# Performance work log

Measured on AMD Instinct MI355X. Metric: run time of the kernel, lower is better.

The kernel has to match this reference:

```python
import jax, jax.numpy as jnp
import numpy as np

# MiniCPM-style decode-step config (matches init_kwargs)
L, B, H, HKV, D, S, HID, FF = 8, 4, 16, 8, 64, 2048, 1024, 2816
SCALE_DEPTH = 1.4
ROPE_THETA = 10000.0
EPS = 1e-5


def _rms(x, w):
    v = jnp.mean(jnp.square(x), axis=-1, keepdims=True)
    return x * jax.lax.rsqrt(v + EPS) * w


def _rotate_half(x):
    x1, x2 = jnp.split(x, 2, axis=-1)
    return jnp.concatenate([-x2, x1], axis=-1)


def setup_inputs() -> dict:
    key = jax.random.key(0)
    ks = jax.random.split(key, 12)
    s = lambda i, shape, fan: jax.random.normal(ks[i], shape, jnp.float32) / np.sqrt(fan)
    return {
        "x": jax.random.normal(ks[0], (B, HID), jnp.float32),
        "k_cache": jax.random.normal(ks[1], (L, B, HKV, S, D), jnp.float32),
        "v_cache": jax.random.normal(ks[2], (L, B, HKV, S, D), jnp.float32),
        "Wq": s(3, (L, HID, H * D), HID),
        "Wk": s(4, (L, HID, HKV * D), HID),
        "Wv": s(5, (L, HID, HKV * D), HID),
        "Wo": s(6, (L, H * D, HID), H * D),
        "Wgate": s(7, (L, HID, FF), HID),
        "Wup": s(8, (L, HID, FF), HID),
        "Wdown": s(9, (L, FF, HID), FF),
        "norm1_w": jnp.ones((L, HID), jnp.float32),
        "norm2_w": jnp.ones((L, HID), jnp.float32),
        "final_norm_w": jnp.ones((HID,), jnp.float32),
        "current_length": 1500,
    }


def reference(x, k_cache, v_cache, Wq, Wk, Wv, Wo, Wgate, Wup, Wdown,
              norm1_w, norm2_w, final_norm_w, current_length):
    pos = jnp.asarray(current_length, jnp.int32)
    # RoPE for the single new position (rope_emb(position_id))
    inv_freq = 1.0 / (ROPE_THETA ** (jnp.arange(0, D, 2, dtype=jnp.float32) / D))
    ang = pos.astype(jnp.float32) * inv_freq            # [D/2]
    cos = jnp.concatenate([jnp.cos(ang), jnp.cos(ang)])  # [D]
    sin = jnp.concatenate([jnp.sin(ang), jnp.sin(ang)])
    positions = jnp.arange(S)
    write_mask = (positions == pos)[None, None, :, None]  # [1,1,S,1]
    valid = (positions <= pos)                            # [S]
    mup = SCALE_DEPTH / np.sqrt(L)
    g = H // HKV

    def layer(h, params):
        wq, wk, wv, wo, wg, wu, wd, n1, n2, kc, vc = params
        hn = _rms(h, n1)
        q = (hn @ wq).reshape(B, HKV, g, 1, D)   # grouped query heads
        k = (hn @ wk).reshape(B, HKV, 1, D)
        v = (hn @ wv).reshape(B, HKV, 1, D)
        q = q * cos + _rotate_half(q) * sin
        k = k * cos + _rotate_half(k) * sin
        # broadcast 'where' write into the full static cache (faithful to source)
        ak = jnp.where(write_mask, k, kc)         # [B,HKV,S,D]
        av = jnp.where(write_mask, v, vc)
        scores = jnp.einsum('bhgqd,bhsd->bhgqs', q, ak) / np.sqrt(D)
        scores = jnp.where(valid[None, None, None, None, :], scores, -jnp.inf)
        p = jax.nn.softmax(scores, axis=-1)
        o = jnp.einsum('bhgqs,bhsd->bhgqd', p, av).reshape(B, H * D)
        h = h + (o @ wo) * mup
        hn2 = _rms(h, n2)
        m = (jax.nn.silu(hn2 @ wg) * (hn2 @ wu)) @ wd
        h = h + m * mup
        return h, (k, v)  # one-position K/V updates [B,HKV,1,D]

    xs = (Wq, Wk, Wv, Wo, Wgate, Wup, Wdown, norm1_w, norm2_w, k_cache, v_cache)
    h, (k_upd, v_upd) = jax.lax.scan(layer, x, xs)
    h = _rms(h, final_norm_w)
    return h, k_upd, v_upd, pos + 1
```

## Files before the change

kernel.cpp:

```cpp
#include <hip/hip_runtime.h>

#define L_   8
#define B_   4
#define H_   16
#define HKV_ 8
#define D_   64
#define S_   2048
#define HID_ 1024
#define FF_  2816
#define EPS_ 1e-5f
#define MUP_ 0.49497474683058327f
#define SCALE_ 0.125f
#define NCH_ 32

#define OUT_H   0
#define OUT_K   4096
#define OUT_V   (4096 + 16384)
#define OUT_POS (4096 + 16384 + 16384)

enum {
  WS_HC  = 0,
  WS_QP  = 4096,
  WS_AM  = WS_QP + 262144,
  WS_AL  = WS_AM + 2048,
  WS_AO  = WS_AL + 2048,
  WS_GP  = WS_AO + 131072,
  WS_UP  = WS_GP + 360448,
  WS_END = WS_UP + 360448
};

__device__ __forceinline__ int read_pos_dev(const int* p) {
  int v = p[0];
  if (v >= 0 && v < S_) return v;
  float f = __int_as_float(v);
  if (f >= 0.0f && f <= (float)(S_ - 1)) return (int)(f + 0.5f);
  return 1500;
}

__device__ __forceinline__ float wave_sum(float v) {
  for (int m = 1; m < 64; m <<= 1) v += __shfl_xor(v, m);
  return v;
}
__device__ __forceinline__ float wave_max(float v) {
  for (int m = 1; m < 64; m <<= 1) v = fmaxf(v, __shfl_xor(v, m));
  return v;
}

__device__ __forceinline__ void rms_of(const float* hsrc, float* red, float* rs) {
  int t = threadIdx.x;
  float part[4] = {0.f, 0.f, 0.f, 0.f};
  #pragma unroll
  for (int j = 0; j < 4; ++j) {
    int c2 = t + j * 256;
    #pragma unroll
    for (int b = 0; b < 4; ++b) {
      float v = hsrc[b * HID_ + c2];
      part[b] += v * v;
    }
  }
  int w = t >> 6;
  #pragma unroll
  for (int b = 0; b < 4; ++b) {
    float s = wave_sum(part[b]);
    if ((t & 63) == 0) red[w * 4 + b] = s;
  }
  __syncthreads();
  #pragma unroll
  for (int b = 0; b < 4; ++b)
    rs[b] = rsqrtf((red[b] + red[4 + b] + red[8 + b] + red[12 + b]) * (1.0f / HID_) + EPS_);
}

__global__ void __launch_bounds__(256)
k1_qkv(const float* __restrict__ Wq, const float* __restrict__ Wk,
       const float* __restrict__ Wv, const float* __restrict__ n1,
       const float* __restrict__ x, float* __restrict__ ws, int l) {
  int cb = blockIdx.x & 7, kc = blockIdx.x >> 3;
  int t = threadIdx.x;
  int col = cb * 256 + t;
  const float* W; int wcol, stride;
  if (col < 1024)      { W = Wq + (size_t)l * HID_ * 1024; wcol = col;        stride = 1024; }
  else if (col < 1536) { W = Wk + (size_t)l * HID_ * 512;  wcol = col - 1024; stride = 512;  }
  else                 { W = Wv + (size_t)l * HID_ * 512;  wcol = col - 1536; stride = 512;  }
  const float* wp = W + (size_t)(kc * 32) * stride + wcol;
  float wv[32];
  #pragma unroll
  for (int i = 0; i < 32; ++i) wv[i] = wp[(size_t)i * stride];

  const float* hsrc = (l == 0) ? x : (ws + WS_HC);
  __shared__ float red[16];
  __shared__ __align__(16) float xs[4][32];
  float rs[4];
  rms_of(hsrc, red, rs);
  if (l == 0 && blockIdx.x < 4) {
    for (int j = 0; j < 4; ++j) {
      int c2 = t + j * 256;
      ws[WS_HC + blockIdx.x * HID_ + c2] = x[blockIdx.x * HID_ + c2];
    }
  }
  if (t < 128) {
    int b = t >> 5, i = t & 31;
    int gc = kc * 32 + i;
    xs[b][i] = hsrc[b * HID_ + gc] * rs[b] * n1[l * HID_ + gc];
  }
  __syncthreads();
  float a0 = 0.f, a1 = 0.f, a2 = 0.f, a3 = 0.f;
  #pragma unroll
  for (int i = 0; i < 32; ++i) {
    float w_ = wv[i];
    a0 += w_ * xs[0][i]; a1 += w_ * xs[1][i];
    a2 += w_ * xs[2][i]; a3 += w_ * xs[3][i];
  }
  ws[WS_QP + ((size_t)kc * 4 + 0) * 2048 + col] = a0;
  ws[WS_QP + ((size_t)kc * 4 + 1) * 2048 + col] = a1;
  ws[WS_QP + ((size_t)kc * 4 + 2) * 2048 + col] = a2;
  ws[WS_QP + ((size_t)kc * 4 + 3) * 2048 + col] = a3;
}

__global__ void __launch_bounds__(256)
k2_attn(const float* __restrict__ kcache, const float* __restrict__ vcache,
        const int* __restrict__ posp, float* __restrict__ ws,
        float* __restrict__ out, int l) {
  int bh = blockIdx.x >> 5, ns = blockIdx.x & 31;
  int b = bh >> 3, kv = bh & 7;
  int t = threadIdx.x;
  int w = t >> 6, lane = t & 63, r = lane >> 4, c = lane & 15;
  int pos = read_pos_dev(posp);
  int s0 = ns * 64;
  if (s0 > pos) {
    if (t == 0) {
      int base = ((b * HKV_ + kv) * 2) * NCH_ + ns;
      ws[WS_AM + base] = -1e30f;       ws[WS_AM + base + NCH_] = -1e30f;
      ws[WS_AL + base] = 0.f;          ws[WS_AL + base + NCH_] = 0.f;
    }
    return;
  }
  __shared__ __align__(16) float Kst[64 * 68];
  __shared__ __align__(16) float Vst[64 * 68];
  __shared__ __align__(16) float qL[2][64];
  __shared__ __align__(16) float knL[64], vnL[64];
  __shared__ float rawL[256], sc0[64], sc1[64], red[8];
  __shared__ __align__(16) float oacc[2][4][64];

  const float* Kb = kcache + (((size_t)l * B_ + b) * HKV_ + kv) * S_ * 64;
  const float* Vb = vcache + (((size_t)l * B_ + b) * HKV_ + kv) * S_ * 64;

  {
    const float4* Ksrc = (const float4*)(Kb + (size_t)s0 * 64);
    const float4* Vsrc = (const float4*)(Vb + (size_t)s0 * 64);
    #pragma unroll
    for (int i = 0; i < 4; ++i) {
      int f4 = t + i * 256;
      int row = f4 >> 4, c4 = f4 & 15;
      float4 kk = Ksrc[f4];
      float4 vv = Vsrc[f4];
      *(float4*)&Kst[row * 68 + 4 * c4] = kk;
      *(float4*)&Vst[row * 68 + 4 * c4] = vv;
    }
  }

  int cg;
  if (t < 128)      cg = (kv * 2 + (t >> 6)) * 64 + (t & 63);
  else if (t < 192) cg = 1024 + kv * 64 + (t & 63);
  else              cg = 1536 + kv * 64 + (t & 63);
  float s = 0.f;
  #pragma unroll
  for (int q = 0; q < 32; ++q) s += ws[WS_QP + ((size_t)q * 4 + b) * 2048 + cg];
  rawL[t] = s;
  __syncthreads();
  {
    int dd = t & 63;
    if (t < 192) {
      int idx = dd & 31;
      float inv = expf(-(float)idx * (1.0f / 32.0f) * 9.210340371976184f);
      float ang = (float)pos * inv;
      float sn, cs; __sincosf(ang, &sn, &cs);
      float partner = rawL[t ^ 32];
      float rot = (dd < 32) ? -partner : partner;
      float v = rawL[t] * cs + rot * sn;
      if (t < 128) qL[t >> 6][dd] = v;
      else {
        knL[dd] = v;
        if (ns == 0) out[OUT_K + (((size_t)l * B_ + b) * HKV_ + kv) * 64 + dd] = v;
      }
    } else {
      vnL[dd] = rawL[t];
      if (ns == 0) out[OUT_V + (((size_t)l * B_ + b) * HKV_ + kv) * 64 + dd] = rawL[t];
    }
  }
  __syncthreads();
  if (pos >= s0 && pos < s0 + 64) {
    int row = pos - s0;
    if (t < 64)                Kst[row * 68 + t] = knL[t];
    else if (t < 128)          Vst[row * 68 + (t - 64)] = vnL[t - 64];
  }
  __syncthreads();

  float4 q0 = *(float4*)&qL[0][4 * c];
  float4 q1 = *(float4*)&qL[1][4 * c];
  #pragma unroll
  for (int it = 0; it < 4; ++it) {
    int row = it * 16 + w * 4 + r;
    int sp = s0 + row;
    float4 k4 = *(float4*)&Kst[row * 68 + 4 * c];
    float d0 = k4.x * q0.x + k4.y * q0.y + k4.z * q0.z + k4.w * q0.w;
    float d1 = k4.x * q1.x + k4.y * q1.y + k4.z * q1.z + k4.w * q1.w;
    #pragma unroll
    for (int m = 1; m <= 8; m <<= 1) { d0 += __shfl_xor(d0, m); d1 += __shfl_xor(d1, m); }
    if (c == 0) {
      bool valid = (sp <= pos);
      sc0[row] = valid ? d0 * SCALE_ : -1e30f;
      sc1[row] = valid ? d1 * SCALE_ : -1e30f;
    }
  }
  __syncthreads();
  float v0 = (t < 64) ? sc0[t] : -1e30f;
  float v1 = (t < 64) ? sc1[t] : -1e30f;
  float m0 = wave_max(v0), m1 = wave_max(v1);
  if (lane == 0) { red[w] = m0; red[4 + w] = m1; }
  __syncthreads();
  m0 = fmaxf(fmaxf(red[0], red[1]), fmaxf(red[2], red[3]));
  m1 = fmaxf(fmaxf(red[4], red[5]), fmaxf(red[6], red[7]));
  float e0 = (t < 64) ? expf(v0 - m0) : 0.f;
  float e1 = (t < 64) ? expf(v1 - m1) : 0.f;
  __syncthreads();
  if (t < 64) { sc0[t] = e0; sc1[t] = e1; }
  float se0 = wave_sum(e0), se1 = wave_sum(e1);
  if (lane == 0) { red[w] = se0; red[4 + w] = se1; }
  __syncthreads();
  if (t == 0) {
    int base = ((b * HKV_ + kv) * 2) * NCH_ + ns;
    ws[WS_AM + base] = m0;          ws[WS_AM + base + NCH_] = m1;
    ws[WS_AL + base] = red[0] + red[1] + red[2] + red[3];
    ws[WS_AL + base + NCH_] = red[4] + red[5] + red[6] + red[7];
  }
  float4 a0 = make_float4(0.f, 0.f, 0.f, 0.f);
  float4 a1 = make_float4(0.f, 0.f, 0.f, 0.f);
  #pragma unroll
  for (int it = 0; it < 4; ++it) {
    int row = it * 16 + w * 4 + r;
    float4 v4 = *(float4*)&Vst[row * 68 + 4 * c];
    float p0 = sc0[row], p1 = sc1[row];
    a0.x += p0 * v4.x; a0.y += p0 * v4.y; a0.z += p0 * v4.z; a0.w += p0 * v4.w;
    a1.x += p1 * v4.x; a1.y += p1 * v4.y; a1.z += p1 * v4.z; a1.w += p1 * v4.w;
  }
  #pragma unroll
  for (int m = 16; m <= 32; m <<= 1) {
    a0.x += __shfl_xor(a0.x, m); a0.y += __shfl_xor(a0.y, m);
    a0.z += __shfl_xor(a0.z, m); a0.w += __shfl_xor(a0.w, m);
    a1.x += __shfl_xor(a1.x, m); a1.y += __shfl_xor(a1.y, m);
    a1.z += __shfl_xor(a1.z, m); a1.w += __shfl_xor(a1.w, m);
  }
  if (r == 0) {
    *(float4*)&oacc[0][w][4 * c] = a0;
    *(float4*)&oacc[1][w][4 * c] = a1;
  }
  __syncthreads();
  if (t < 64) {
    float r0 = oacc[0][0][t] + oacc[0][1][t] + oacc[0][2][t] + oacc[0][3][t];
    float r1 = oacc[1][0][t] + oacc[1][1][t] + oacc[1][2][t] + oacc[1][3][t];
    int h0 = kv * 2;
    ws[WS_AO + ((size_t)(b * H_ + h0)     * NCH_ + ns) * 64 + t] = r0;
    ws[WS_AO + ((size_t)(b * H_ + h0 + 1) * NCH_ + ns) * 64 + t] = r1;
  }
}

__global__ void __launch_bounds__(256)
k3_oproj(const float* __restrict__ Wo, float* __restrict__ ws, int l) {
  int cb = blockIdx.x & 3, kc = blockIdx.x >> 2;
  int t = threadIdx.x;
  int col = cb * 256 + t;
  const float* wp = Wo + ((size_t)l * HID_ + kc * 16) * HID_ + col;
  float wv[16];
  #pragma unroll
  for (int i = 0; i < 16; ++i) wv[i] = wp[(size_t)i * HID_];

  __shared__ __align__(16) float oT[16][4];
  if (t < 64) {
    int jj = t >> 2, bb = t & 3;
    int dim = kc * 16 + jj, h = dim >> 6, d = dim & 63;
    int mb = ((bb * HKV_ + (h >> 1)) * 2 + (h & 1)) * NCH_;
    float mx = -1e30f;
    #pragma unroll
    for (int n = 0; n < NCH_; ++n) mx = fmaxf(mx, ws[WS_AM + mb + n]);
    float ls = 0.f, os = 0.f;
    #pragma unroll
    for (int n = 0; n < NCH_; ++n) {
      float wg = expf(ws[WS_AM + mb + n] - mx);
      ls += wg * ws[WS_AL + mb + n];
      os += wg * ws[WS_AO + ((size_t)(bb * H_ + h) * NCH_ + n) * 64 + d];
    }
    oT[jj][bb] = os / ls;
  }
  __syncthreads();
  float a0 = 0.f, a1 = 0.f, a2 = 0.f, a3 = 0.f;
  #pragma unroll
  for (int i = 0; i < 16; ++i) {
    float w_ = wv[i];
    float4 o4 = *(float4*)&oT[i][0];
    a0 += w_ * o4.x; a1 += w_ * o4.y; a2 += w_ * o4.z; a3 += w_ * o4.w;
  }
  atomicAdd(ws + WS_HC + 0 * HID_ + col, MUP_ * a0);
  atomicAdd(ws + WS_HC + 1 * HID_ + col, MUP_ * a1);
  atomicAdd(ws + WS_HC + 2 * HID_ + col, MUP_ * a2);
  atomicAdd(ws + WS_HC + 3 * HID_ + col, MUP_ * a3);
}

__global__ void __launch_bounds__(256)
k4_gateup(const float* __restrict__ Wg, const float* __restrict__ Wu,
          const float* __restrict__ n2, float* __restrict__ ws, int l) {
  int cb = blockIdx.x % 11, kc = blockIdx.x / 11;
  int t = threadIdx.x;
  int col = cb * 256 + t;
  const float* wgp = Wg + ((size_t)l * HID_ + kc * 32) * FF_ + col;
  const float* wup = Wu + ((size_t)l * HID_ + kc * 32) * FF_ + col;
  float gv[32], uv[32];
  #pragma unroll
  for (int i = 0; i < 32; ++i) { gv[i] = wgp[(size_t)i * FF_]; uv[i] = wup[(size_t)i * FF_]; }

  const float* hsrc = ws + WS_HC;
  __shared__ float red[16];
  __shared__ __align__(16) float xs[4][32];
  float rs[4];
  rms_of(hsrc, red, rs);
  if (t < 128) {
    int b = t >> 5, i = t & 31;
    int gc = kc * 32 + i;
    xs[b][i] = hsrc[b * HID_ + gc] * rs[b] * n2[l * HID_ + gc];
  }
  __syncthreads();
  float g0 = 0.f, g1 = 0.f, g2 = 0.f, g3 = 0.f;
  float u0 = 0.f, u1 = 0.f, u2 = 0.f, u3 = 0.f;
  #pragma unroll
  for (int i = 0; i < 32; ++i) {
    float g = gv[i], u = uv[i];
    float x0 = xs[0][i], x1 = xs[1][i], x2 = xs[2][i], x3 = xs[3][i];
    g0 += g * x0; g1 += g * x1; g2 += g * x2; g3 += g * x3;
    u0 += u * x0; u1 += u * x1; u2 += u * x2; u3 += u * x3;
  }
  ws[WS_GP + ((size_t)kc * 4 + 0) * FF_ + col] = g0;
  ws[WS_GP + ((size_t)kc * 4 + 1) * FF_ + col] = g1;
  ws[WS_GP + ((size_t)kc * 4 + 2) * FF_ + col] = g2;
  ws[WS_GP + ((size_t)kc * 4 + 3) * FF_ + col] = g3;
  ws[WS_UP + ((size_t)kc * 4 + 0) * FF_ + col] = u0;
  ws[WS_UP + ((size_t)kc * 4 + 1) * FF_ + col] = u1;
  ws[WS_UP + ((size_t)kc * 4 + 2) * FF_ + col] = u2;
  ws[WS_UP + ((size_t)kc * 4 + 3) * FF_ + col] = u3;
}

__global__ void __launch_bounds__(256)
k5_down(const float* __restrict__ Wd, float* __restrict__ ws, int l) {
  int cb = blockIdx.x & 3, kc = blockIdx.x >> 2;
  int t = threadIdx.x;
  int col = cb * 256 + t;
  const float* wp = Wd + ((size_t)l * FF_ + kc * 32) * HID_ + col;
  float wv[32];
  #pragma unroll
  for (int i = 0; i < 32; ++i) wv[i] = wp[(size_t)i * HID_];

  __shared__ __align__(16) float mT[32][4];
  if (t < 128) {
    int jj = t >> 2, bb = t & 3;
    int f = kc * 32 + jj;
    float g = 0.f, u = 0.f;
    #pragma unroll
    for (int k2 = 0; k2 < 32; ++k2) {
      g += ws[WS_GP + ((size_t)k2 * 4 + bb) * FF_ + f];
      u += ws[WS_UP + ((size_t)k2 * 4 + bb) * FF_ + f];
    }
    float sig = 1.f / (1.f + expf(-g));
    mT[jj][bb] = g * sig * u;
  }
  __syncthreads();
  float a0 = 0.f, a1 = 0.f, a2 = 0.f, a3 = 0.f;
  #pragma unroll
  for (int i = 0; i < 32; ++i) {
    float w_ = wv[i];
    float4 m4 = *(float4*)&mT[i][0];
    a0 += w_ * m4.x; a1 += w_ * m4.y; a2 += w_ * m4.z; a3 += w_ * m4.w;
  }
  atomicAdd(ws + WS_HC + 0 * HID_ + col, MUP_ * a0);
  atomicAdd(ws + WS_HC + 1 * HID_ + col, MUP_ * a1);
  atomicAdd(ws + WS_HC + 2 * HID_ + col, MUP_ * a2);
  atomicAdd(ws + WS_HC + 3 * HID_ + col, MUP_ * a3);
}

__global__ void __launch_bounds__(256)
k6_final(const float* __restrict__ fw, const int* __restrict__ posp,
         float* __restrict__ ws, float* __restrict__ out) {
  int b = blockIdx.x, t = threadIdx.x;
  __shared__ float red[4];
  float hv[4];
  float part = 0.f;
  for (int j = 0; j < 4; ++j) {
    float v = ws[WS_HC + b * HID_ + t + j * 256];
    hv[j] = v; part += v * v;
  }
  part = wave_sum(part);
  if ((t & 63) == 0) red[t >> 6] = part;
  __syncthreads();
  float rs = rsqrtf((red[0] + red[1] + red[2] + red[3]) * (1.0f / HID_) + EPS_);
  for (int j = 0; j < 4; ++j) {
    int c2 = t + j * 256;
    out[OUT_H + b * HID_ + c2] = hv[j] * rs * fw[c2];
  }
  if (b == 0 && t == 0) out[OUT_POS] = (float)(read_pos_dev(posp) + 1);
}

extern "C" void kernel_launch(void* const* d_in, const int* in_sizes, int n_in,
                              void* d_out, int out_size, void* d_ws, size_t ws_size,
                              hipStream_t stream) {
  const float* x   = (const float*)d_in[0];
  const float* kcp = (const float*)d_in[1];
  const float* vcp = (const float*)d_in[2];
  const float* Wq  = (const float*)d_in[3];
  const float* Wk  = (const float*)d_in[4];
  const float* Wv  = (const float*)d_in[5];
  const float* Wo  = (const float*)d_in[6];
  const float* Wg  = (const float*)d_in[7];
  const float* Wu  = (const float*)d_in[8];
  const float* Wd  = (const float*)d_in[9];
  const float* n1  = (const float*)d_in[10];
  const float* n2  = (const float*)d_in[11];
  const float* fw  = (const float*)d_in[12];
  const int*   pos = (const int*)d_in[13];
  float* ws  = (float*)d_ws;
  float* out = (float*)d_out;

  for (int l = 0; l < L_; ++l) {
    k1_qkv   <<< 256, 256, 0, stream>>>(Wq, Wk, Wv, n1, x, ws, l);
    k2_attn  <<<1024, 256, 0, stream>>>(kcp, vcp, pos, ws, out, l);
    k3_oproj <<< 256, 256, 0, stream>>>(Wo, ws, l);
    k4_gateup<<< 352, 256, 0, stream>>>(Wg, Wu, n2, ws, l);
    k5_down  <<< 352, 256, 0, stream>>>(Wd, ws, l);
  }
  k6_final<<<4, 256, 0, stream>>>(fw, pos, ws, out);
}
```

Before: 324.4 us.

## Prefetch next kernel's weights and KV cache into L2 from the preceding kernel

Each kernel now issues dummy loads, one per 64-byte cache line, covering the data the next kernel in the chain will read: k1 touches the K/V cache tiles for attention, k2 touches Wo, k3 touches Wgate/Wup, k4 touches Wdown, and k5 touches the next layer's Wq/Wk/Wv. An empty asm keeps the loaded values alive so the compiler does not remove the loads. The aim is to warm L2/MALL so the following launch finds its data in cache and hides the DRAM latency of a memory-bound decode step. The cost is extra memory traffic and register pressure inside each kernel. If the cache cannot hold the prefetched data until the next kernel runs, the loads are wasted.

Measured after the change: 320.7 us. About the same (-1.1%).

```diff
diff --git a/kernel.cpp b/kernel.cpp
--- a/kernel.cpp
+++ b/kernel.cpp
@@ -45,6 +45,7 @@
   for (int m = 1; m < 64; m <<= 1) v = fmaxf(v, __shfl_xor(v, m));
   return v;
 }
+__device__ __forceinline__ void keepf(float v) { asm volatile("" :: "v"(v)); }
 
 __device__ __forceinline__ void rms_of(const float* hsrc, float* red, float* rs) {
   int t = threadIdx.x;
@@ -73,7 +74,9 @@
 __global__ void __launch_bounds__(256)
 k1_qkv(const float* __restrict__ Wq, const float* __restrict__ Wk,
        const float* __restrict__ Wv, const float* __restrict__ n1,
-       const float* __restrict__ x, float* __restrict__ ws, int l) {
+       const float* __restrict__ x, const float* __restrict__ kcache,
+       const float* __restrict__ vcache, const int* __restrict__ posp,
+       float* __restrict__ ws, int l) {
   int cb = blockIdx.x & 7, kc = blockIdx.x >> 3;
   int t = threadIdx.x;
   int col = cb * 256 + t;
@@ -102,6 +105,23 @@
     int gc = kc * 32 + i;
     xs[b][i] = hsrc[b * HID_ + gc] * rs[b] * n1[l * HID_ + gc];
   }
+
+  int pos = read_pos_dev(posp);
+  float pf[8];
+  {
+    int row = t >> 2, off = (t & 3) * 16;
+    #pragma unroll
+    for (int m = 0; m < 4; ++m) {
+      int j = blockIdx.x + m * 256;
+      int bh2 = j >> 5, ns2 = j & 31;
+      int s02 = ns2 * 64;
+      bool act = (s02 <= pos);
+      size_t base = (((size_t)l * B_ + (bh2 >> 3)) * HKV_ + (bh2 & 7)) * S_ * 64
+                  + (size_t)(s02 + row) * 64 + off;
+      pf[2 * m + 0] = act ? kcache[base] : 0.f;
+      pf[2 * m + 1] = act ? vcache[base] : 0.f;
+    }
+  }
   __syncthreads();
   float a0 = 0.f, a1 = 0.f, a2 = 0.f, a3 = 0.f;
   #pragma unroll
@@ -114,24 +134,35 @@
   ws[WS_QP + ((size_t)kc * 4 + 1) * 2048 + col] = a1;
   ws[WS_QP + ((size_t)kc * 4 + 2) * 2048 + col] = a2;
   ws[WS_QP + ((size_t)kc * 4 + 3) * 2048 + col] = a3;
+  #pragma unroll
+  for (int m = 0; m < 8; ++m) keepf(pf[m]);
 }
 
 __global__ void __launch_bounds__(256)
 k2_attn(const float* __restrict__ kcache, const float* __restrict__ vcache,
-        const int* __restrict__ posp, float* __restrict__ ws,
-        float* __restrict__ out, int l) {
+        const int* __restrict__ posp, const float* __restrict__ Wo,
+        float* __restrict__ ws, float* __restrict__ out, int l) {
   int bh = blockIdx.x >> 5, ns = blockIdx.x & 31;
   int b = bh >> 3, kv = bh & 7;
   int t = threadIdx.x;
   int w = t >> 6, lane = t & 63, r = lane >> 4, c = lane & 15;
   int pos = read_pos_dev(posp);
   int s0 = ns * 64;
+
+  float pfo = 0.f;
+  if (blockIdx.x < 256) {
+    int cb3 = blockIdx.x & 3, kc3 = blockIdx.x >> 2;
+    int r3 = t >> 4, c3 = (t & 15) * 16;
+    pfo = Wo[((size_t)l * HID_ + kc3 * 16 + r3) * HID_ + cb3 * 256 + c3];
+  }
+
   if (s0 > pos) {
     if (t == 0) {
       int base = ((b * HKV_ + kv) * 2) * NCH_ + ns;
       ws[WS_AM + base] = -1e30f;       ws[WS_AM + base + NCH_] = -1e30f;
       ws[WS_AL + base] = 0.f;          ws[WS_AL + base + NCH_] = 0.f;
     }
+    keepf(pfo);
     return;
   }
   __shared__ __align__(16) float Kst[64 * 68];
@@ -262,10 +293,12 @@
     ws[WS_AO + ((size_t)(b * H_ + h0)     * NCH_ + ns) * 64 + t] = r0;
     ws[WS_AO + ((size_t)(b * H_ + h0 + 1) * NCH_ + ns) * 64 + t] = r1;
   }
+  keepf(pfo);
 }
 
 __global__ void __launch_bounds__(256)
-k3_oproj(const float* __restrict__ Wo, float* __restrict__ ws, int l) {
+k3_oproj(const float* __restrict__ Wo, const float* __restrict__ Wg,
+         const float* __restrict__ Wu, float* __restrict__ ws, int l) {
   int cb = blockIdx.x & 3, kc = blockIdx.x >> 2;
   int t = threadIdx.x;
   int col = cb * 256 + t;
@@ -291,6 +324,25 @@
     }
     oT[jj][bb] = os / ls;
   }
+
+  float pf[8];
+  {
+    #pragma unroll
+    for (int rg = 0; rg < 2; ++rg) {
+      int j = blockIdx.x + rg * 256;
+      bool act = (j < 352);
+      int jj2 = act ? j : 0;
+      int cb4 = jj2 % 11, kc4 = jj2 / 11;
+      #pragma unroll
+      for (int q = 0; q < 2; ++q) {
+        int m = t + q * 256;
+        int r4 = m >> 4, c4 = (m & 15) * 16;
+        size_t o4 = ((size_t)l * HID_ + kc4 * 32 + r4) * FF_ + cb4 * 256 + c4;
+        pf[rg * 4 + q * 2 + 0] = act ? Wg[o4] : 0.f;
+        pf[rg * 4 + q * 2 + 1] = act ? Wu[o4] : 0.f;
+      }
+    }
+  }
   __syncthreads();
   float a0 = 0.f, a1 = 0.f, a2 = 0.f, a3 = 0.f;
   #pragma unroll
@@ -303,11 +355,14 @@
   atomicAdd(ws + WS_HC + 1 * HID_ + col, MUP_ * a1);
   atomicAdd(ws + WS_HC + 2 * HID_ + col, MUP_ * a2);
   atomicAdd(ws + WS_HC + 3 * HID_ + col, MUP_ * a3);
+  #pragma unroll
+  for (int m = 0; m < 8; ++m) keepf(pf[m]);
 }
 
 __global__ void __launch_bounds__(256)
 k4_gateup(const float* __restrict__ Wg, const float* __restrict__ Wu,
-          const float* __restrict__ n2, float* __restrict__ ws, int l) {
+          const float* __restrict__ Wd, const float* __restrict__ n2,
+          float* __restrict__ ws, int l) {
   int cb = blockIdx.x % 11, kc = blockIdx.x / 11;
   int t = threadIdx.x;
   int col = cb * 256 + t;
@@ -327,6 +382,17 @@
     int gc = kc * 32 + i;
     xs[b][i] = hsrc[b * HID_ + gc] * rs[b] * n2[l * HID_ + gc];
   }
+
+  float pf[2];
+  {
+    int cb5 = blockIdx.x & 3, kc5 = blockIdx.x >> 2;
+    #pragma unroll
+    for (int q = 0; q < 2; ++q) {
+      int m = t + q * 256;
+      int r5 = m >> 4, c5 = (m & 15) * 16;
+      pf[q] = Wd[((size_t)l * FF_ + kc5 * 32 + r5) * HID_ + cb5 * 256 + c5];
+    }
+  }
   __syncthreads();
   float g0 = 0.f, g1 = 0.f, g2 = 0.f, g3 = 0.f;
   float u0 = 0.f, u1 = 0.f, u2 = 0.f, u3 = 0.f;
@@ -345,10 +411,13 @@
   ws[WS_UP + ((size_t)kc * 4 + 1) * FF_ + col] = u1;
   ws[WS_UP + ((size_t)kc * 4 + 2) * FF_ + col] = u2;
   ws[WS_UP + ((size_t)kc * 4 + 3) * FF_ + col] = u3;
+  keepf(pf[0]); keepf(pf[1]);
 }
 
 __global__ void __launch_bounds__(256)
-k5_down(const float* __restrict__ Wd, float* __restrict__ ws, int l) {
+k5_down(const float* __restrict__ Wd, const float* __restrict__ Wq,
+        const float* __restrict__ Wk, const float* __restrict__ Wv,
+        float* __restrict__ ws, int l) {
   int cb = blockIdx.x & 3, kc = blockIdx.x >> 2;
   int t = threadIdx.x;
   int col = cb * 256 + t;
@@ -370,6 +439,22 @@
     float sig = 1.f / (1.f + expf(-g));
     mT[jj][bb] = g * sig * u;
   }
+
+  float pf[2] = {0.f, 0.f};
+  if (l + 1 < L_ && blockIdx.x < 256) {
+    int cb1 = blockIdx.x & 7, kc1 = blockIdx.x >> 3;
+    #pragma unroll
+    for (int q = 0; q < 2; ++q) {
+      int m = t + q * 256;
+      int r1 = m >> 4, c1 = (m & 15) * 16;
+      int pcol = cb1 * 256 + c1;
+      const float* W1; int wcol1, stride1;
+      if (pcol < 1024)      { W1 = Wq + (size_t)(l + 1) * HID_ * 1024; wcol1 = pcol;        stride1 = 1024; }
+      else if (pcol < 1536) { W1 = Wk + (size_t)(l + 1) * HID_ * 512;  wcol1 = pcol - 1024; stride1 = 512;  }
+      else                  { W1 = Wv + (size_t)(l + 1) * HID_ * 512;  wcol1 = pcol - 1536; stride1 = 512;  }
+      pf[q] = W1[(size_t)(kc1 * 32 + r1) * stride1 + wcol1];
+    }
+  }
   __syncthreads();
   float a0 = 0.f, a1 = 0.f, a2 = 0.f, a3 = 0.f;
   #pragma unroll
@@ -382,6 +467,7 @@
   atomicAdd(ws + WS_HC + 1 * HID_ + col, MUP_ * a1);
   atomicAdd(ws + WS_HC + 2 * HID_ + col, MUP_ * a2);
   atomicAdd(ws + WS_HC + 3 * HID_ + col, MUP_ * a3);
+  keepf(pf[0]); keepf(pf[1]);
 }
 
 __global__ void __launch_bounds__(256)
@@ -427,11 +513,11 @@
   float* out = (float*)d_out;
 
   for (int l = 0; l < L_; ++l) {
-    k1_qkv   <<< 256, 256, 0, stream>>>(Wq, Wk, Wv, n1, x, ws, l);
-    k2_attn  <<<1024, 256, 0, stream>>>(kcp, vcp, pos, ws, out, l);
-    k3_oproj <<< 256, 256, 0, stream>>>(Wo, ws, l);
-    k4_gateup<<< 352, 256, 0, stream>>>(Wg, Wu, n2, ws, l);
-    k5_down  <<< 352, 256, 0, stream>>>(Wd, ws, l);
+    k1_qkv   <<< 256, 256, 0, stream>>>(Wq, Wk, Wv, n1, x, kcp, vcp, pos, ws, l);
+    k2_attn  <<<1024, 256, 0, stream>>>(kcp, vcp, pos, Wo, ws, out, l);
+    k3_oproj <<< 256, 256, 0, stream>>>(Wo, Wg, Wu, ws, l);
+    k4_gateup<<< 352, 256, 0, stream>>>(Wg, Wu, Wd, n2, ws, l);
+    k5_down  <<< 352, 256, 0, stream>>>(Wd, Wq, Wk, Wv, ws, l);
   }
   k6_final<<<4, 256, 0, stream>>>(fw, pos, ws, out);
 }
```

## Fuse all layers into one persistent cooperative megakernel with flag-based stage sync

Applied to the files above, without the earlier changes.

Replaces the 41 separate kernel launches with a single persistent 512-block kernel. Stages and layers are ordered by atomic counters in the workspace, and each stage is spin-waited on before it proceeds. Weight and KV-cache loads are issued before each wait so that memory traffic overlaps the previous stage. Per-layer workspace planes avoid write-after-read hazards, and the residual is kept in interleaved buffers. This removes launch overhead and tail bubbles, but it risks deadlock if not all blocks are resident (there is a timed-out spin) and it adds atomic contention.

After: 1.106 ms. 241% more time.

```diff
diff --git a/kernel.cpp b/kernel.cpp
--- a/kernel.cpp
+++ b/kernel.cpp
@@ -18,6 +18,481 @@
 #define OUT_V   (4096 + 16384)
 #define OUT_POS (4096 + 16384 + 16384)
 
+#define PL_QP   0
+#define PL_AM   262144
+#define PL_AL   263168
+#define PL_AO   264192
+#define PL_HCA  395264
+#define PL_HCB  399360
+#define PL_GP   403456
+#define PL_UP   763904
+#define PL_SZ   1124352
+#define FL_BASE (8 * PL_SZ)
+#define NEED_FLOATS (FL_BASE + 1024)
+#define FI(l,k) (((l) * 5 + (k)) * 16)
+
+__device__ __forceinline__ int read_pos_dev(const int* p) {
+  int v = p[0];
+  if (v >= 0 && v < S_) return v;
+  float f = __int_as_float(v);
+  if (f >= 0.0f && f <= (float)(S_ - 1)) return (int)(f + 0.5f);
+  return 1500;
+}
+__device__ __forceinline__ float wave_sum(float v) {
+  for (int m = 1; m < 64; m <<= 1) v += __shfl_xor(v, m);
+  return v;
+}
+__device__ __forceinline__ float wave_max(float v) {
+  for (int m = 1; m < 64; m <<= 1) v = fmaxf(v, __shfl_xor(v, m));
+  return v;
+}
+__device__ __forceinline__ void stg_a(float* p, float v) {
+  __hip_atomic_store(p, v, __ATOMIC_RELAXED, __HIP_MEMORY_SCOPE_AGENT);
+}
+__device__ __forceinline__ void fwait(int* flg, int idx, int target) {
+  if (threadIdx.x == 0) {
+    int n = 0;
+    while (__hip_atomic_load(flg + idx, __ATOMIC_RELAXED,
+                             __HIP_MEMORY_SCOPE_AGENT) < target) {
+      __builtin_amdgcn_s_sleep(32);
+      if (++n > (1 << 22)) break;
+    }
+  }
+  __syncthreads();
+}
+__device__ __forceinline__ void fadd(int* flg, int idx) {
+  if (threadIdx.x == 0) atomicAdd(flg + idx, 1);
+}
+
+__global__ void k_init(float* ws) {
+  int i = blockIdx.x * 256 + threadIdx.x;
+  if (i < 1024) ((int*)(ws + FL_BASE))[i] = 0;
+}
+
+__global__ void __launch_bounds__(256, 2)
+mega(const float* __restrict__ kcache, const float* __restrict__ vcache,
+     const float* __restrict__ Wq, const float* __restrict__ Wk,
+     const float* __restrict__ Wv, const float* __restrict__ Wo,
+     const float* __restrict__ Wg, const float* __restrict__ Wu,
+     const float* __restrict__ Wd, const float* __restrict__ n1,
+     const float* __restrict__ n2, const float* __restrict__ fw,
+     const float* __restrict__ x, const int* __restrict__ posp,
+     float* ws, float* out) {
+  const int bid = blockIdx.x, t = threadIdx.x;
+  int* flg = (int*)(ws + FL_BASE);
+  const int pos = read_pos_dev(posp);
+  __shared__ __align__(16) float smem[9872];
+
+  if (bid == 4 && t == 0) out[OUT_POS] = (float)(pos + 1);
+
+  #pragma unroll 1
+  for (int l = 0; l < L_; ++l) {
+    float* qp_  = ws + (size_t)l * PL_SZ + PL_QP;
+    float* am_  = ws + (size_t)l * PL_SZ + PL_AM;
+    float* al_  = ws + (size_t)l * PL_SZ + PL_AL;
+    float* ao_  = ws + (size_t)l * PL_SZ + PL_AO;
+    float* hca_ = ws + (size_t)l * PL_SZ + PL_HCA;
+    float* hcb_ = ws + (size_t)l * PL_SZ + PL_HCB;
+    float* gp_  = ws + (size_t)l * PL_SZ + PL_GP;
+    float* up_  = ws + (size_t)l * PL_SZ + PL_UP;
+
+    if (bid < 256) {
+      int cb = bid & 7, kc = bid >> 3;
+      int col = cb * 256 + t;
+      const float* W; int wcol, stride;
+      if (col < 1024)      { W = Wq + (size_t)l * HID_ * 1024; wcol = col;        stride = 1024; }
+      else if (col < 1536) { W = Wk + (size_t)l * HID_ * 512;  wcol = col - 1024; stride = 512;  }
+      else                 { W = Wv + (size_t)l * HID_ * 512;  wcol = col - 1536; stride = 512;  }
+      const float* wp = W + (size_t)(kc * 32) * stride + wcol;
+      float wv[32];
+      #pragma unroll
+      for (int i = 0; i < 32; ++i) wv[i] = wp[(size_t)i * stride];
+
+      if (l > 0) fwait(flg, FI(l - 1, 4), 352);
+
+      const float* hcbp = ws + (size_t)(l - 1) * PL_SZ + PL_HCB;
+      float4 h4[4];
+      #pragma unroll
+      for (int j = 0; j < 4; ++j) {
+        int c2 = t + j * 256;
+        if (l == 0) h4[j] = make_float4(x[c2], x[1024 + c2], x[2048 + c2], x[3072 + c2]);
+        else        h4[j] = *(const float4*)&hcbp[c2 * 4];
+      }
+      float part[4] = {0.f, 0.f, 0.f, 0.f};
+      #pragma unroll
+      for (int j = 0; j < 4; ++j) {
+        part[0] += h4[j].x * h4[j].x; part[1] += h4[j].y * h4[j].y;
+        part[2] += h4[j].z * h4[j].z; part[3] += h4[j].w * h4[j].w;
+      }
+      float* red = smem;
+      float* xs  = smem + 16;
+      int w_ = t >> 6;
+      #pragma unroll
+      for (int b = 0; b < 4; ++b) {
+        float s = wave_sum(part[b]);
+        if ((t & 63) == 0) red[w_ * 4 + b] = s;
+      }
+      __syncthreads();
+      float rs[4];
+      #pragma unroll
+      for (int b = 0; b < 4; ++b)
+        rs[b] = rsqrtf((red[b] + red[4 + b] + red[8 + b] + red[12 + b]) * (1.0f / HID_) + EPS_);
+      if (bid < 4) {
+        #pragma unroll
+        for (int j = 0; j < 4; ++j) {
+          int c2 = t + j * 256;
+          float v = (bid == 0) ? h4[j].x : (bid == 1) ? h4[j].y : (bid == 2) ? h4[j].z : h4[j].w;
+          stg_a(hca_ + c2 * 4 + bid, v);
+        }
+      }
+      if (t < 128) {
+        int b = t >> 5, i = t & 31;
+        int gc = kc * 32 + i;
+        float hval = (l == 0) ? x[b * HID_ + gc] : hcbp[gc * 4 + b];
+        xs[b * 32 + i] = hval * rs[b] * n1[l * HID_ + gc];
+      }
+      __syncthreads();
+      float a0 = 0.f, a1 = 0.f, a2 = 0.f, a3 = 0.f;
+      #pragma unroll
+      for (int i = 0; i < 32; ++i) {
+        float w = wv[i];
+        a0 += w * xs[i]; a1 += w * xs[32 + i];
+        a2 += w * xs[64 + i]; a3 += w * xs[96 + i];
+      }
+      stg_a(qp_ + ((size_t)(0 * 2048 + col)) * 32 + kc, a0);
+      stg_a(qp_ + ((size_t)(1 * 2048 + col)) * 32 + kc, a1);
+      stg_a(qp_ + ((size_t)(2 * 2048 + col)) * 32 + kc, a2);
+      stg_a(qp_ + ((size_t)(3 * 2048 + col)) * 32 + kc, a3);
+      __syncthreads();
+      fadd(flg, FI(l, 0));
+    }
+
+    {
+      int w = t >> 6, lane = t & 63, r = lane >> 4, c = lane & 15;
+      float* Kst = smem;          float* Vst = smem + 4352;
+      float* qL  = smem + 8704;   float* knL = smem + 8832;
+      float* vnL = smem + 8896;   float* rawL = smem + 8960;
+      float* sA  = smem + 9216;   float* sB  = smem + 9280;
+      float* red = smem + 9344;   float* oacc = smem + 9360;
+
+      float4 kr[4], vr[4];
+      {
+        int cid = bid, bh = cid >> 5, ns = cid & 31, s0 = ns * 64;
+        if (s0 <= pos) {
+          const float4* Ks = (const float4*)(kcache + (((size_t)l * B_ + (bh >> 3)) * HKV_ + (bh & 7)) * S_ * 64 + (size_t)s0 * 64);
+          const float4* Vs = (const float4*)(vcache + (((size_t)l * B_ + (bh >> 3)) * HKV_ + (bh & 7)) * S_ * 64 + (size_t)s0 * 64);
+          #pragma unroll
+          for (int i = 0; i < 4; ++i) { int f4 = t + i * 256; kr[i] = Ks[f4]; vr[i] = Vs[f4]; }
+        }
+      }
+      fwait(flg, FI(l, 0), 256);
+
+      #pragma unroll 1
+      for (int sub = 0; sub < 2; ++sub) {
+        int cid = bid + sub * 512;
+        int bh = cid >> 5, ns = cid & 31;
+        int b = bh >> 3, kv = bh & 7;
+        int s0 = ns * 64;
+        if (sub == 1 && s0 <= pos) {
+          const float4* Ks = (const float4*)(kcache + (((size_t)l * B_ + b) * HKV_ + kv) * S_ * 64 + (size_t)s0 * 64);
+          const float4* Vs = (const float4*)(vcache + (((size_t)l * B_ + b) * HKV_ + kv) * S_ * 64 + (size_t)s0 * 64);
+          #pragma unroll
+          for (int i = 0; i < 4; ++i) { int f4 = t + i * 256; kr[i] = Ks[f4]; vr[i] = Vs[f4]; }
+        }
+        if (s0 > pos) {
+          if (t == 0) {
+            int base = ((b * HKV_ + kv) * 2) * 32 + ns;
+            stg_a(am_ + base, -1e30f);        stg_a(am_ + base + 32, -1e30f);
+            stg_a(al_ + base, 0.f);           stg_a(al_ + base + 32, 0.f);
+          }
+        } else {
+          #pragma unroll
+          for (int i = 0; i < 4; ++i) {
+            int f4 = t + i * 256;
+            int row = f4 >> 4, c4 = f4 & 15;
+            *(float4*)&Kst[row * 68 + 4 * c4] = kr[i];
+            *(float4*)&Vst[row * 68 + 4 * c4] = vr[i];
+          }
+          int cg;
+          if (t < 128)      cg = (kv * 2 + (t >> 6)) * 64 + (t & 63);
+          else if (t < 192) cg = 1024 + kv * 64 + (t & 63);
+          else              cg = 1536 + kv * 64 + (t & 63);
+          const float* qpp = qp_ + ((size_t)(b * 2048 + cg)) * 32;
+          float s = 0.f;
+          #pragma unroll
+          for (int q = 0; q < 32; ++q) s += qpp[q];
+          rawL[t] = s;
+          __syncthreads();
+          {
+            int dd = t & 63;
+            if (t < 192) {
+              int idx = dd & 31;
+              float inv = expf(-(float)idx * (1.0f / 32.0f) * 9.210340371976184f);
+              float ang = (float)pos * inv;
+              float sn, cs; __sincosf(ang, &sn, &cs);
+              float partner = rawL[t ^ 32];
+              float rot = (dd < 32) ? -partner : partner;
+              float v = rawL[t] * cs + rot * sn;
+              if (t < 128) qL[(t >> 6) * 64 + dd] = v;
+              else {
+                knL[dd] = v;
+                if (ns == 0) out[OUT_K + (((size_t)l * B_ + b) * HKV_ + kv) * 64 + dd] = v;
+              }
+            } else {
+              vnL[dd] = rawL[t];
+              if (ns == 0) out[OUT_V + (((size_t)l * B_ + b) * HKV_ + kv) * 64 + dd] = rawL[t];
+            }
+          }
+          __syncthreads();
+          if (pos >= s0 && pos < s0 + 64) {
+            int row = pos - s0;
+            if (t < 64)       Kst[row * 68 + t] = knL[t];
+            else if (t < 128) Vst[row * 68 + (t - 64)] = vnL[t - 64];
+          }
+          __syncthreads();
+          float4 q0 = *(float4*)&qL[4 * c];
+          float4 q1 = *(float4*)&qL[64 + 4 * c];
+          #pragma unroll
+          for (int it = 0; it < 4; ++it) {
+            int row = it * 16 + w * 4 + r;
+            int sp = s0 + row;
+            float4 k4 = *(float4*)&Kst[row * 68 + 4 * c];
+            float d0 = k4.x * q0.x + k4.y * q0.y + k4.z * q0.z + k4.w * q0.w;
+            float d1 = k4.x * q1.x + k4.y * q1.y + k4.z * q1.z + k4.w * q1.w;
+            #pragma unroll
+            for (int m = 1; m <= 8; m <<= 1) { d0 += __shfl_xor(d0, m); d1 += __shfl_xor(d1, m); }
+            if (c == 0) {
+              bool valid = (sp <= pos);
+              sA[row] = valid ? d0 * SCALE_ : -1e30f;
+              sB[row] = valid ? d1 * SCALE_ : -1e30f;
+            }
+          }
+          __syncthreads();
+          float v0 = (t < 64) ? sA[t] : -1e30f;
+          float v1 = (t < 64) ? sB[t] : -1e30f;
+          float m0 = wave_max(v0), m1 = wave_max(v1);
+          if (lane == 0) { red[w] = m0; red[4 + w] = m1; }
+          __syncthreads();
+          m0 = fmaxf(fmaxf(red[0], red[1]), fmaxf(red[2], red[3]));
+          m1 = fmaxf(fmaxf(red[4], red[5]), fmaxf(red[6], red[7]));
+          float e0 = (t < 64) ? expf(v0 - m0) : 0.f;
+          float e1 = (t < 64) ? expf(v1 - m1) : 0.f;
+          __syncthreads();
+          if (t < 64) { sA[t] = e0; sB[t] = e1; }
+          float se0 = wave_sum(e0), se1 = wave_sum(e1);
+          if (lane == 0) { red[w] = se0; red[4 + w] = se1; }
+          __syncthreads();
+          if (t == 0) {
+            int base = ((b * HKV_ + kv) * 2) * 32 + ns;
+            stg_a(am_ + base, m0);          stg_a(am_ + base + 32, m1);
+            stg_a(al_ + base, red[0] + red[1] + red[2] + red[3]);
+            stg_a(al_ + base + 32, red[4] + red[5] + red[6] + red[7]);
+          }
+          float4 a0 = make_float4(0.f, 0.f, 0.f, 0.f);
+          float4 a1 = make_float4(0.f, 0.f, 0.f, 0.f);
+          #pragma unroll
+          for (int it = 0; it < 4; ++it) {
+            int row = it * 16 + w * 4 + r;
+            float4 v4 = *(float4*)&Vst[row * 68 + 4 * c];
+            float p0 = sA[row], p1 = sB[row];
+            a0.x += p0 * v4.x; a0.y += p0 * v4.y; a0.z += p0 * v4.z; a0.w += p0 * v4.w;
+            a1.x += p1 * v4.x; a1.y += p1 * v4.y; a1.z += p1 * v4.z; a1.w += p1 * v4.w;
+          }
+          #pragma unroll
+          for (int m = 16; m <= 32; m <<= 1) {
+            a0.x += __shfl_xor(a0.x, m); a0.y += __shfl_xor(a0.y, m);
+            a0.z += __shfl_xor(a0.z, m); a0.w += __shfl_xor(a0.w, m);
+            a1.x += __shfl_xor(a1.x, m); a1.y += __shfl_xor(a1.y, m);
+            a1.z += __shfl_xor(a1.z, m); a1.w += __shfl_xor(a1.w, m);
+          }
+          if (r == 0) {
+            *(float4*)&oacc[w * 64 + 4 * c] = a0;
+            *(float4*)&oacc[256 + w * 64 + 4 * c] = a1;
+          }
+          __syncthreads();
+          if (t < 64) {
+            float r0 = oacc[t] + oacc[64 + t] + oacc[128 + t] + oacc[192 + t];
+            float r1 = oacc[256 + t] + oacc[320 + t] + oacc[384 + t] + oacc[448 + t];
+            int h0 = kv * 2;
+            stg_a(ao_ + (((size_t)(b * 16 + h0))     * 64 + t) * 32 + ns, r0);
+            stg_a(ao_ + (((size_t)(b * 16 + h0 + 1)) * 64 + t) * 32 + ns, r1);
+          }
+        }
+        __syncthreads();
+      }
+      fadd(flg, FI(l, 1));
+    }
+
+    if (bid < 256) {
+      int cb = bid & 3, kc = bid >> 2;
+      int col = cb * 256 + t;
+      const float* wp = Wo + ((size_t)l * HID_ + kc * 16) * HID_ + col;
+      float wv[16];
+      #pragma unroll
+      for (int i = 0; i < 16; ++i) wv[i] = wp[(size_t)i * HID_];
+      fwait(flg, FI(l, 1), 512);
+      float* oT = smem;
+      if (t < 64) {
+        int jj = t >> 2, bb = t & 3;
+        int dim = kc * 16 + jj, h = dim >> 6, d = dim & 63;
+        const float* amp = am_ + ((bb * 8 + (h >> 1)) * 2 + (h & 1)) * 32;
+        const float* alp = al_ + ((bb * 8 + (h >> 1)) * 2 + (h & 1)) * 32;
+        const float* aop = ao_ + (((size_t)(bb * 16 + h)) * 64 + d) * 32;
+        float mx = -1e30f;
+        #pragma unroll
+        for (int n = 0; n < 32; ++n) mx = fmaxf(mx, amp[n]);
+        float ls = 0.f, os = 0.f;
+        #pragma unroll
+        for (int n = 0; n < 32; ++n) {
+          float wg = expf(amp[n] - mx);
+          ls += wg * alp[n];
+          os += wg * aop[n];
+        }
+        oT[jj * 4 + bb] = os / ls;
+      }
+      __syncthreads();
+      float a0 = 0.f, a1 = 0.f, a2 = 0.f, a3 = 0.f;
+      #pragma unroll
+      for (int i = 0; i < 16; ++i) {
+        float w = wv[i];
+        a0 += w * oT[i * 4 + 0]; a1 += w * oT[i * 4 + 1];
+        a2 += w * oT[i * 4 + 2]; a3 += w * oT[i * 4 + 3];
+      }
+      atomicAdd(hca_ + col * 4 + 0, MUP_ * a0);
+      atomicAdd(hca_ + col * 4 + 1, MUP_ * a1);
+      atomicAdd(hca_ + col * 4 + 2, MUP_ * a2);
+      atomicAdd(hca_ + col * 4 + 3, MUP_ * a3);
+      __syncthreads();
+      fadd(flg, FI(l, 2));
+    }
+
+    if (bid < 352) {
+      int cb = bid % 11, kc = bid / 11;
+      int col = cb * 256 + t;
+      const float* wgp = Wg + ((size_t)l * HID_ + kc * 32) * FF_ + col;
+      const float* wup = Wu + ((size_t)l * HID_ + kc * 32) * FF_ + col;
+      float gv[32], uv[32];
+      #pragma unroll
+      for (int i = 0; i < 32; ++i) { gv[i] = wgp[(size_t)i * FF_]; uv[i] = wup[(size_t)i * FF_]; }
+      fwait(flg, FI(l, 2), 256);
+      float4 h4[4];
+      #pragma unroll
+      for (int j = 0; j < 4; ++j) h4[j] = *(const float4*)&hca_[(t + j * 256) * 4];
+      float part[4] = {0.f, 0.f, 0.f, 0.f};
+      #pragma unroll
+      for (int j = 0; j < 4; ++j) {
+        part[0] += h4[j].x * h4[j].x; part[1] += h4[j].y * h4[j].y;
+        part[2] += h4[j].z * h4[j].z; part[3] += h4[j].w * h4[j].w;
+      }
+      float* red = smem;
+      float* xs  = smem + 16;
+      int w_ = t >> 6;
+      #pragma unroll
+      for (int b = 0; b < 4; ++b) {
+        float s = wave_sum(part[b]);
+        if ((t & 63) == 0) red[w_ * 4 + b] = s;
+      }
+      __syncthreads();
+      float rs[4];
+      #pragma unroll
+      for (int b = 0; b < 4; ++b)
+        rs[b] = rsqrtf((red[b] + red[4 + b] + red[8 + b] + red[12 + b]) * (1.0f / HID_) + EPS_);
+      if (bid < 4) {
+        #pragma unroll
+        for (int j = 0; j < 4; ++j) {
+          int c2 = t + j * 256;
+          float v = (bid == 0) ? h4[j].x : (bid == 1) ? h4[j].y : (bid == 2) ? h4[j].z : h4[j].w;
+          stg_a(hcb_ + c2 * 4 + bid, v);
+        }
+      }
+      if (t < 128) {
+        int b = t >> 5, i = t & 31;
+        int gc = kc * 32 + i;
+        xs[b * 32 + i] = hca_[gc * 4 + b] * rs[b] * n2[l * HID_ + gc];
+      }
+      __syncthreads();
+      float g0 = 0.f, g1 = 0.f, g2 = 0.f, g3 = 0.f;
+      float u0 = 0.f, u1 = 0.f, u2 = 0.f, u3 = 0.f;
+      #pragma unroll
+      for (int i = 0; i < 32; ++i) {
+        float g = gv[i], u = uv[i];
+        float x0 = xs[i], x1 = xs[32 + i], x2 = xs[64 + i], x3 = xs[96 + i];
+        g0 += g * x0; g1 += g * x1; g2 += g * x2; g3 += g * x3;
+        u0 += u * x0; u1 += u * x1; u2 += u * x2; u3 += u * x3;
+      }
+      stg_a(gp_ + ((size_t)(0 * FF_ + col)) * 32 + kc, g0);
+      stg_a(gp_ + ((size_t)(1 * FF_ + col)) * 32 + kc, g1);
+      stg_a(gp_ + ((size_t)(2 * FF_ + col)) * 32 + kc, g2);
+      stg_a(gp_ + ((size_t)(3 * FF_ + col)) * 32 + kc, g3);
+      stg_a(up_ + ((size_t)(0 * FF_ + col)) * 32 + kc, u0);
+      stg_a(up_ + ((size_t)(1 * FF_ + col)) * 32 + kc, u1);
+      stg_a(up_ + ((size_t)(2 * FF_ + col)) * 32 + kc, u2);
+      stg_a(up_ + ((size_t)(3 * FF_ + col)) * 32 + kc, u3);
+      __syncthreads();
+      fadd(flg, FI(l, 3));
+    }
+
+    if (bid < 352) {
+      int cb = bid & 3, kc = bid >> 2;
+      int col = cb * 256 + t;
+      const float* wp = Wd + ((size_t)l * FF_ + kc * 32) * HID_ + col;
+      float wv[32];
+      #pragma unroll
+      for (int i = 0; i < 32; ++i) wv[i] = wp[(size_t)i * HID_];
+      fwait(flg, FI(l, 3), 352);
+      float* mT = smem;
+      if (t < 128) {
+        int jj = t >> 2, bb = t & 3;
+        int f = kc * 32 + jj;
+        const float* gpp = gp_ + ((size_t)(bb * FF_ + f)) * 32;
+        const float* upp = up_ + ((size_t)(bb * FF_ + f)) * 32;
+        float g = 0.f, u = 0.f;
+        #pragma unroll
+        for (int q = 0; q < 32; ++q) { g += gpp[q]; u += upp[q]; }
+        float sig = 1.f / (1.f + expf(-g));
+        mT[jj * 4 + bb] = g * sig * u;
+      }
+      __syncthreads();
+      float a0 = 0.f, a1 = 0.f, a2 = 0.f, a3 = 0.f;
+      #pragma unroll
+      for (int i = 0; i < 32; ++i) {
+        float w = wv[i];
+        a0 += w * mT[i * 4 + 0]; a1 += w * mT[i * 4 + 1];
+        a2 += w * mT[i * 4 + 2]; a3 += w * mT[i * 4 + 3];
+      }
+      atomicAdd(hcb_ + col * 4 + 0, MUP_ * a0);
+      atomicAdd(hcb_ + col * 4 + 1, MUP_ * a1);
+      atomicAdd(hcb_ + col * 4 + 2, MUP_ * a2);
+      atomicAdd(hcb_ + col * 4 + 3, MUP_ * a3);
+      __syncthreads();
+      fadd(flg, FI(l, 4));
+    }
+  }
+
+  if (bid < 4) {
+    fwait(flg, FI(L_ - 1, 4), 352);
+    const float* hcb7 = ws + (size_t)(L_ - 1) * PL_SZ + PL_HCB;
+    int b = bid;
+    float* red = smem;
+    float hv[4];
+    float part = 0.f;
+    #pragma unroll
+    for (int j = 0; j < 4; ++j) {
+      float v = hcb7[(t + j * 256) * 4 + b];
+      hv[j] = v; part += v * v;
+    }
+    part = wave_sum(part);
+    if ((t & 63) == 0) red[t >> 6] = part;
+    __syncthreads();
+    float rs = rsqrtf((red[0] + red[1] + red[2] + red[3]) * (1.0f / HID_) + EPS_);
+    #pragma unroll
+    for (int j = 0; j < 4; ++j) {
+      int c2 = t + j * 256;
+      out[OUT_H + b * HID_ + c2] = hv[j] * rs * fw[c2];
+    }
+  }
+}
+
 enum {
   WS_HC  = 0,
   WS_QP  = 4096,
@@ -29,23 +504,6 @@
   WS_END = WS_UP + 360448
 };
 
-__device__ __forceinline__ int read_pos_dev(const int* p) {
-  int v = p[0];
-  if (v >= 0 && v < S_) return v;
-  float f = __int_as_float(v);
-  if (f >= 0.0f && f <= (float)(S_ - 1)) return (int)(f + 0.5f);
-  return 1500;
-}
-
-__device__ __forceinline__ float wave_sum(float v) {
-  for (int m = 1; m < 64; m <<= 1) v += __shfl_xor(v, m);
-  return v;
-}
-__device__ __forceinline__ float wave_max(float v) {
-  for (int m = 1; m < 64; m <<= 1) v = fmaxf(v, __shfl_xor(v, m));
-  return v;
-}
-
 __device__ __forceinline__ void rms_of(const float* hsrc, float* red, float* rs) {
   int t = threadIdx.x;
   float part[4] = {0.f, 0.f, 0.f, 0.f};
@@ -53,10 +511,7 @@
   for (int j = 0; j < 4; ++j) {
     int c2 = t + j * 256;
     #pragma unroll
-    for (int b = 0; b < 4; ++b) {
-      float v = hsrc[b * HID_ + c2];
-      part[b] += v * v;
-    }
+    for (int b = 0; b < 4; ++b) { float v = hsrc[b * HID_ + c2]; part[b] += v * v; }
   }
   int w = t >> 6;
   #pragma unroll
@@ -85,7 +540,6 @@
   float wv[32];
   #pragma unroll
   for (int i = 0; i < 32; ++i) wv[i] = wp[(size_t)i * stride];
-
   const float* hsrc = (l == 0) ? x : (ws + WS_HC);
   __shared__ float red[16];
   __shared__ __align__(16) float xs[4][32];
@@ -140,10 +594,8 @@
   __shared__ __align__(16) float knL[64], vnL[64];
   __shared__ float rawL[256], sc0[64], sc1[64], red[8];
   __shared__ __align__(16) float oacc[2][4][64];
-
   const float* Kb = kcache + (((size_t)l * B_ + b) * HKV_ + kv) * S_ * 64;
   const float* Vb = vcache + (((size_t)l * B_ + b) * HKV_ + kv) * S_ * 64;
-
   {
     const float4* Ksrc = (const float4*)(Kb + (size_t)s0 * 64);
     const float4* Vsrc = (const float4*)(Vb + (size_t)s0 * 64);
@@ -157,7 +609,6 @@
       *(float4*)&Vst[row * 68 + 4 * c4] = vv;
     }
   }
-
   int cg;
   if (t < 128)      cg = (kv * 2 + (t >> 6)) * 64 + (t & 63);
   else if (t < 192) cg = 1024 + kv * 64 + (t & 63);
@@ -190,11 +641,10 @@
   __syncthreads();
   if (pos >= s0 && pos < s0 + 64) {
     int row = pos - s0;
-    if (t < 64)                Kst[row * 68 + t] = knL[t];
-    else if (t < 128)          Vst[row * 68 + (t - 64)] = vnL[t - 64];
-  }
-  __syncthreads();
-
+    if (t < 64)       Kst[row * 68 + t] = knL[t];
+    else if (t < 128) Vst[row * 68 + (t - 64)] = vnL[t - 64];
+  }
+  __syncthreads();
   float4 q0 = *(float4*)&qL[0][4 * c];
   float4 q1 = *(float4*)&qL[1][4 * c];
   #pragma unroll
@@ -273,7 +723,6 @@
   float wv[16];
   #pragma unroll
   for (int i = 0; i < 16; ++i) wv[i] = wp[(size_t)i * HID_];
-
   __shared__ __align__(16) float oT[16][4];
   if (t < 64) {
     int jj = t >> 2, bb = t & 3;
@@ -316,7 +765,6 @@
   float gv[32], uv[32];
   #pragma unroll
   for (int i = 0; i < 32; ++i) { gv[i] = wgp[(size_t)i * FF_]; uv[i] = wup[(size_t)i * FF_]; }
-
   const float* hsrc = ws + WS_HC;
   __shared__ float red[16];
   __shared__ __align__(16) float xs[4][32];
@@ -356,7 +804,6 @@
   float wv[32];
   #pragma unroll
   for (int i = 0; i < 32; ++i) wv[i] = wp[(size_t)i * HID_];
-
   __shared__ __align__(16) float mT[32][4];
   if (t < 128) {
     int jj = t >> 2, bb = t & 3;
@@ -426,12 +873,26 @@
   float* ws  = (float*)d_ws;
   float* out = (float*)d_out;
 
-  for (int l = 0; l < L_; ++l) {
-    k1_qkv   <<< 256, 256, 0, stream>>>(Wq, Wk, Wv, n1, x, ws, l);
-    k2_attn  <<<1024, 256, 0, stream>>>(kcp, vcp, pos, ws, out, l);
-    k3_oproj <<< 256, 256, 0, stream>>>(Wo, ws, l);
-    k4_gateup<<< 352, 256, 0, stream>>>(Wg, Wu, n2, ws, l);
-    k5_down  <<< 352, 256, 0, stream>>>(Wd, ws, l);
-  }
-  k6_final<<<4, 256, 0, stream>>>(fw, pos, ws, out);
-}
+  if (ws_size >= (size_t)NEED_FLOATS * sizeof(float)) {
+    k_init<<<4, 256, 0, stream>>>(ws);
+    void* args[] = { (void*)&kcp, (void*)&vcp, (void*)&Wq, (void*)&Wk, (void*)&Wv,
+                     (void*)&Wo, (void*)&Wg, (void*)&Wu, (void*)&Wd, (void*)&n1,
+                     (void*)&n2, (void*)&fw, (void*)&x, (void*)&pos,
+                     (void*)&ws, (void*)&out };
+    hipError_t e = hipLaunchCooperativeKernel((const void*)mega, dim3(512), dim3(256),
+                                              args, 0, stream);
+    if (e != hipSuccess) {
+      mega<<<512, 256, 0, stream>>>(kcp, vcp, Wq, Wk, Wv, Wo, Wg, Wu, Wd,
+                                    n1, n2, fw, x, pos, ws, out);
+    }
+  } else {
+    for (int l = 0; l < L_; ++l) {
+      k1_qkv   <<< 256, 256, 0, stream>>>(Wq, Wk, Wv, n1, x, ws, l);
+      k2_attn  <<<1024, 256, 0, stream>>>(kcp, vcp, pos, ws, out, l);
+      k3_oproj <<< 256, 256, 0, stream>>>(Wo, ws, l);
+      k4_gateup<<< 352, 256, 0, stream>>>(Wg, Wu, n2, ws, l);
+      k5_down  <<< 352, 256, 0, stream>>>(Wd, ws, l);
+    }
+    k6_final<<<4, 256, 0, stream>>>(fw, pos, ws, out);
+  }
+}
```
